# Optimization experiments

Hardware: AMD Instinct MI355X
Metric: run time of the kernel (lower is better)

Reference implementation:

```python
import jax, jax.numpy as jnp
import numpy as np

THRESH = 0.6
MIN_KEPT = 200000
FACTOR = 8
IGNORE_LABEL = -1


def _lin_coords(n_in, n_out):
    # scipy.ndimage.zoom (grid_mode=False): input_coord = i * (n_in-1)/(n_out-1)
    return jnp.linspace(0.0, n_in - 1.0, n_out)


def _zoom_bilinear(x, h_out, w_out):
    # x: (n, c, h, w) -> (n, c, h_out, w_out), separable order-1 (bilinear) zoom
    h, w = x.shape[-2], x.shape[-1]
    yc = _lin_coords(h, h_out)
    xc = _lin_coords(w, w_out)
    y0 = jnp.floor(yc).astype(jnp.int32)
    y1 = jnp.minimum(y0 + 1, h - 1)
    wy = (yc - y0)[None, None, :, None]
    x0 = jnp.floor(xc).astype(jnp.int32)
    x1 = jnp.minimum(x0 + 1, w - 1)
    wx = xc - x0
    a = jnp.take(x, y0, axis=2) * (1.0 - wy) + jnp.take(x, y1, axis=2) * wy
    return jnp.take(a, x0, axis=3) * (1.0 - wx) + jnp.take(a, x1, axis=3) * wx


def _zoom_nearest(t, h_out, w_out):
    # t: (n, h, w) int labels -> (n, h_out, w_out), order-0 (nearest) zoom
    h, w = t.shape[-2], t.shape[-1]
    yi = jnp.round(_lin_coords(h, h_out)).astype(jnp.int32)
    xi = jnp.round(_lin_coords(w, w_out)).astype(jnp.int32)
    return t[:, yi][:, :, xi]


def setup_inputs() -> dict:
    key = jax.random.key(0)
    k1, k2 = jax.random.split(key)
    predict = jax.random.normal(k1, (8, 19, 512, 1024), dtype=jnp.float32)
    target = jax.random.randint(k2, (8, 512, 1024), 0, 19, dtype=jnp.int32)
    return {"predict": predict, "target": target}


def reference(predict, target):
    n, c, h, w = predict.shape
    prob = jax.nn.softmax(predict, axis=1)  # (n, c, h, w)

    # ---- find_threshold: quantile on the factor-downsampled prediction ----
    h_s, w_s = int(round(h / FACTOR)), int(round(w / FACTOR))
    prob_s = _zoom_bilinear(prob, h_s, w_s)          # (n, c, h_s, w_s)
    tgt_s = _zoom_nearest(target, h_s, w_s)          # (n, h_s, w_s)
    # pred_s[i] = prob_s[n_i, label_i, y_i, x_i]
    pred_s = jnp.take_along_axis(prob_s, tgt_s[:, None].astype(jnp.int32), axis=1)[:, 0].ravel()
    min_kept_s = MIN_KEPT // (FACTOR * FACTOR)
    k_th = min(int(pred_s.shape[0]), min_kept_s) - 1  # static
    kth_val = jnp.sort(pred_s)[k_th]                  # == np.partition(pred, k_th)[k_th]
    threshold = jnp.where(kth_val > THRESH, kth_val, jnp.float32(THRESH))

    # ---- generate_new_target: keep hard pixels (pred prob <= threshold) ----
    pred_full = jnp.take_along_axis(prob, target[:, None].astype(jnp.int32), axis=1)[:, 0]  # (n, h, w)
    kept = (pred_full <= threshold) & (target >= 0)
    new_target = jnp.where(kept, target, IGNORE_LABEL)
    return new_target
```

## Files before the change

### kernel.cpp

```cpp
#include <hip/hip_runtime.h>
#include <math.h>

#define N_IMG 8
#define C_CH 19
#define H_IMG 512
#define W_IMG 1024
#define HW (H_IMG * W_IMG)
#define NDS (N_IMG * 64 * 128)
#define K_TH 3124
#define THRESH_F 0.6f

typedef float  f32x4 __attribute__((ext_vector_type(4)));
typedef int    i32x4 __attribute__((ext_vector_type(4)));

__global__ __launch_bounds__(256) void k0_zero(float* __restrict__ pred_s) {
    int idx = (blockIdx.x * 256 + threadIdx.x) * 4;
    *reinterpret_cast<f32x4*>(pred_s + idx) = (f32x4)(0.0f);
}

__global__ __launch_bounds__(256) void k1_fused(const float* __restrict__ predict,
                                                const int* __restrict__ target,
                                                float* __restrict__ pred_full,
                                                float* __restrict__ pred_s) {
    int tid = blockIdx.x * blockDim.x + threadIdx.x;
    int p = tid * 4;
    int n = p >> 19;
    int o = p & (HW - 1);
    int y = o >> 10;
    int xb = o & 1023;
    const float* base = predict + (size_t)n * C_CH * HW + o;

    i32x4 tg = *reinterpret_cast<const i32x4*>(target + p);

    f32x4 v[C_CH];
    f32x4 m = (f32x4)(-INFINITY);
    #pragma unroll
    for (int c = 0; c < C_CH; c++) {
        f32x4 x = __builtin_nontemporal_load(
            reinterpret_cast<const f32x4*>(base + (size_t)c * HW));
        v[c] = x;
        m.x = fmaxf(m.x, x.x); m.y = fmaxf(m.y, x.y);
        m.z = fmaxf(m.z, x.z); m.w = fmaxf(m.w, x.w);
    }
    f32x4 s = (f32x4)(0.0f);
    f32x4 et = (f32x4)(0.0f);
    #pragma unroll
    for (int c = 0; c < C_CH; c++) {
        float ex = expf(v[c].x - m.x);
        float ey = expf(v[c].y - m.y);
        float ez = expf(v[c].z - m.z);
        float ew = expf(v[c].w - m.w);
        s.x += ex; s.y += ey; s.z += ez; s.w += ew;
        if (c == tg.x) et.x = ex;
        if (c == tg.y) et.y = ey;
        if (c == tg.z) et.z = ez;
        if (c == tg.w) et.w = ew;
    }
    f32x4 pf;
    pf.x = et.x / s.x; pf.y = et.y / s.y; pf.z = et.z / s.z; pf.w = et.w / s.w;
    *reinterpret_cast<f32x4*>(pred_full + p) = pf;

    int jm[2]; float wym[2]; int yrow[2]; int nym = 0;
    {
        int jc = (int)((float)y * (63.0f / 511.0f));
        for (int dj = -1; dj <= 2; dj++) {
            int j = jc + dj;
            if (j < 0 || j > 63) continue;
            float yc = (float)j * (511.0f / 63.0f);
            int y0 = (int)yc;
            if (y0 > H_IMG - 1) y0 = H_IMG - 1;
            int y1 = min(y0 + 1, H_IMG - 1);
            float wy = yc - (float)y0;
            int yi = min((int)rintf(yc), H_IMG - 1);
            if (y0 == y && nym < 2) { jm[nym] = j; wym[nym] = 1.0f - wy; yrow[nym] = yi; nym++; }
            if (y1 == y && nym < 2) { jm[nym] = j; wym[nym] = wy;        yrow[nym] = yi; nym++; }
        }
    }
    if (nym) {
        #pragma unroll
        for (int k = 0; k < 4; k++) {
            int x = xb + k;
            int im[2]; float wxm[2]; int xcol[2]; int nxm = 0;
            int ic = (int)((float)x * (127.0f / 1023.0f));
            for (int di = -1; di <= 2; di++) {
                int i = ic + di;
                if (i < 0 || i > 127) continue;
                float xc = (float)i * (1023.0f / 127.0f);
                int x0 = (int)xc;
                if (x0 > W_IMG - 1) x0 = W_IMG - 1;
                int x1 = min(x0 + 1, W_IMG - 1);
                float wx = xc - (float)x0;
                int xi = min((int)rintf(xc), W_IMG - 1);
                if (x0 == x && nxm < 2) { im[nxm] = i; wxm[nxm] = 1.0f - wx; xcol[nxm] = xi; nxm++; }
                if (x1 == x && nxm < 2) { im[nxm] = i; wxm[nxm] = wx;        xcol[nxm] = xi; nxm++; }
            }
            for (int a = 0; a < nym; a++) {
                for (int b = 0; b < nxm; b++) {
                    int L = target[n * HW + yrow[a] * W_IMG + xcol[b]];
                    if (L < 0) L = 0;
                    float vL = v[0][k];
                    #pragma unroll
                    for (int c = 1; c < C_CH; c++) if (c == L) vL = v[c][k];
                    float e = expf(vL - m[k]);
                    float contrib = wym[a] * wxm[b] * (e / s[k]);
                    atomicAdd(&pred_s[n * 8192 + jm[a] * 128 + im[b]], contrib);
                }
            }
        }
    }
}

#define K2_THREADS 1024
#define K2_WAVES (K2_THREADS / 64)

__global__ __launch_bounds__(K2_THREADS) void k2_select(const float* __restrict__ pred_s,
                                                        float* __restrict__ thr_out) {
    __shared__ unsigned int hist[K2_WAVES * 2048];
    __shared__ unsigned int tot[2048];
    __shared__ unsigned int wsum[K2_WAVES];
    __shared__ unsigned int s_bin, s_k;

    const int t = threadIdx.x;
    const int lane = t & 63;
    const int wave = t >> 6;

    unsigned int prefix = 0;
    unsigned int k = K_TH;

    for (int lvl = 0; lvl < 3; lvl++) {
        const int nb = (lvl == 2) ? 1024 : 2048;

        for (int b = t; b < K2_WAVES * nb; b += K2_THREADS) hist[b] = 0;
        __syncthreads();

        unsigned int* myhist = &hist[wave * nb];
        for (int idx = t; idx < NDS; idx += K2_THREADS) {
            unsigned int u = __float_as_uint(pred_s[idx]);
            bool ok;
            unsigned int bin;
            if (lvl == 0)      { ok = true;                bin = u >> 21; }
            else if (lvl == 1) { ok = (u >> 21) == prefix; bin = (u >> 10) & 2047u; }
            else               { ok = (u >> 10) == prefix; bin = u & 1023u; }
            if (ok) atomicAdd(&myhist[bin], 1u);
        }
        __syncthreads();

        for (int b = t; b < nb; b += K2_THREADS) {
            unsigned int sm = 0;
            #pragma unroll
            for (int w = 0; w < K2_WAVES; w++) sm += hist[w * nb + b];
            tot[b] = sm;
        }
        __syncthreads();

        unsigned int c0, c1, s;
        if (nb == 2048) { c0 = tot[2 * t]; c1 = tot[2 * t + 1]; s = c0 + c1; }
        else            { c0 = tot[t];     c1 = 0;              s = c0; }

        unsigned int incl = s;
        #pragma unroll
        for (int off = 1; off < 64; off <<= 1) {
            unsigned int vv = (unsigned int)__shfl_up((int)incl, off, 64);
            if (lane >= off) incl += vv;
        }
        if (lane == 63) wsum[wave] = incl;
        __syncthreads();
        unsigned int woff = 0;
        for (int w = 0; w < wave; w++) woff += wsum[w];
        unsigned int excl = woff + incl - s;

        if (k >= excl && k < excl + s) {
            if (nb == 2048) {
                if (k < excl + c0) { s_bin = 2u * t;     s_k = k - excl; }
                else               { s_bin = 2u * t + 1; s_k = k - excl - c0; }
            } else {
                s_bin = (unsigned int)t; s_k = k - excl;
            }
        }
        __syncthreads();

        unsigned int b = s_bin;
        k = s_k;
        if (lvl == 0)      prefix = b;
        else if (lvl == 1) prefix = (prefix << 11) | b;
        else               prefix = (prefix << 10) | b;
        __syncthreads();
    }

    if (t == 0) {
        float kth = __uint_as_float(prefix);
        *thr_out = (kth > THRESH_F) ? kth : THRESH_F;
    }
}

__global__ __launch_bounds__(256) void k3_mask(const float* __restrict__ pred_full,
                                               const int* __restrict__ target,
                                               const float* __restrict__ thr_ptr,
                                               int* __restrict__ out) {
    int tid = blockIdx.x * blockDim.x + threadIdx.x;
    int p = tid * 4;
    f32x4 pf = *reinterpret_cast<const f32x4*>(pred_full + p);
    i32x4 tg = *reinterpret_cast<const i32x4*>(target + p);
    float thr = *thr_ptr;
    i32x4 r;
    r.x = (pf.x <= thr && tg.x >= 0) ? tg.x : -1;
    r.y = (pf.y <= thr && tg.y >= 0) ? tg.y : -1;
    r.z = (pf.z <= thr && tg.z >= 0) ? tg.z : -1;
    r.w = (pf.w <= thr && tg.w >= 0) ? tg.w : -1;
    __builtin_nontemporal_store(r, reinterpret_cast<i32x4*>(out + p));
}

extern "C" void kernel_launch(void* const* d_in, const int* in_sizes, int n_in,
                              void* d_out, int out_size, void* d_ws, size_t ws_size,
                              hipStream_t stream) {
    const float* predict = (const float*)d_in[0];
    const int* target    = (const int*)d_in[1];
    int* out = (int*)d_out;

    float* thr       = (float*)d_ws;
    float* pred_s    = (float*)((char*)d_ws + 4096);
    float* pred_full = (float*)((char*)d_ws + (1 << 20));

    hipLaunchKernelGGL(k0_zero, dim3(NDS / (256 * 4)), dim3(256), 0, stream, pred_s);
    hipLaunchKernelGGL(k1_fused, dim3(N_IMG * HW / (4 * 256)), dim3(256), 0, stream,
                       predict, target, pred_full, pred_s);
    hipLaunchKernelGGL(k2_select, dim3(1), dim3(K2_THREADS), 0, stream, pred_s, thr);
    hipLaunchKernelGGL(k3_mask, dim3(N_IMG * HW / (4 * 256)), dim3(256), 0, stream,
                       pred_full, target, thr, out);
}
```

Baseline: 472.8 us.

## Compute downsampled probabilities by direct gather instead of scatter atomics

Replaces the scatter-style accumulation, where full-resolution threads atomically added weighted contributions into the downsampled buffer, with dedicated gather blocks. Each gather thread recomputes softmax at its four bilinear source pixels and writes its downsampled value directly. This drops the zeroing kernel, the atomics and the per-pixel neighbour search in the main path. The cost is redundant softmax work on scattered, uncoalesced strided loads in the gather blocks. Those blocks come first in the grid and may delay the main blocks somewhat.

```diff
diff --git a/kernel.cpp b/kernel.cpp
--- a/kernel.cpp
+++ b/kernel.cpp
@@ -10,24 +10,73 @@
 #define K_TH 3124
 #define THRESH_F 0.6f
 
+#define GATHER_BLOCKS 256
+#define MAIN_BLOCKS (N_IMG * HW / (4 * 256))
+
 typedef float  f32x4 __attribute__((ext_vector_type(4)));
 typedef int    i32x4 __attribute__((ext_vector_type(4)));
-
-__global__ __launch_bounds__(256) void k0_zero(float* __restrict__ pred_s) {
-    int idx = (blockIdx.x * 256 + threadIdx.x) * 4;
-    *reinterpret_cast<f32x4*>(pred_s + idx) = (f32x4)(0.0f);
-}
 
 __global__ __launch_bounds__(256) void k1_fused(const float* __restrict__ predict,
                                                 const int* __restrict__ target,
                                                 float* __restrict__ pred_full,
                                                 float* __restrict__ pred_s) {
-    int tid = blockIdx.x * blockDim.x + threadIdx.x;
+    if (blockIdx.x < GATHER_BLOCKS) {
+        int gid = blockIdx.x * 256 + threadIdx.x;
+        int i = gid & 127;
+        int j = (gid >> 7) & 63;
+        int n = gid >> 13;
+
+        float yc = (float)j * (511.0f / 63.0f);
+        int y0 = (int)yc; if (y0 > H_IMG - 1) y0 = H_IMG - 1;
+        int y1 = min(y0 + 1, H_IMG - 1);
+        float wy = yc - (float)y0;
+        int yi = min((int)rintf(yc), H_IMG - 1);
+
+        float xc = (float)i * (1023.0f / 127.0f);
+        int x0 = (int)xc; if (x0 > W_IMG - 1) x0 = W_IMG - 1;
+        int x1 = min(x0 + 1, W_IMG - 1);
+        float wx = xc - (float)x0;
+        int xi = min((int)rintf(xc), W_IMG - 1);
+
+        int L = target[n * HW + yi * W_IMG + xi];
+        if (L < 0) L = 0;
+
+        const float* basep = predict + (size_t)n * C_CH * HW;
+        float p[2][2];
+        #pragma unroll
+        for (int a = 0; a < 2; a++) {
+            int y = a ? y1 : y0;
+            #pragma unroll
+            for (int b = 0; b < 2; b++) {
+                int x = b ? x1 : x0;
+                const float* bp = basep + y * W_IMG + x;
+                float v[C_CH];
+                float m = -INFINITY;
+                #pragma unroll
+                for (int c = 0; c < C_CH; c++) {
+                    v[c] = bp[(size_t)c * HW];
+                    m = fmaxf(m, v[c]);
+                }
+                float s = 0.0f, eL = 0.0f;
+                #pragma unroll
+                for (int c = 0; c < C_CH; c++) {
+                    float e = expf(v[c] - m);
+                    s += e;
+                    if (c == L) eL = e;
+                }
+                p[a][b] = eL / s;
+            }
+        }
+        float a0 = p[0][0] * (1.0f - wy) + p[1][0] * wy;
+        float a1 = p[0][1] * (1.0f - wy) + p[1][1] * wy;
+        pred_s[n * 8192 + j * 128 + i] = a0 * (1.0f - wx) + a1 * wx;
+        return;
+    }
+
+    int tid = (blockIdx.x - GATHER_BLOCKS) * 256 + threadIdx.x;
     int p = tid * 4;
     int n = p >> 19;
     int o = p & (HW - 1);
-    int y = o >> 10;
-    int xb = o & 1023;
     const float* base = predict + (size_t)n * C_CH * HW + o;
 
     i32x4 tg = *reinterpret_cast<const i32x4*>(target + p);
@@ -59,55 +108,6 @@
     f32x4 pf;
     pf.x = et.x / s.x; pf.y = et.y / s.y; pf.z = et.z / s.z; pf.w = et.w / s.w;
     *reinterpret_cast<f32x4*>(pred_full + p) = pf;
-
-    int jm[2]; float wym[2]; int yrow[2]; int nym = 0;
-    {
-        int jc = (int)((float)y * (63.0f / 511.0f));
-        for (int dj = -1; dj <= 2; dj++) {
-            int j = jc + dj;
-            if (j < 0 || j > 63) continue;
-            float yc = (float)j * (511.0f / 63.0f);
-            int y0 = (int)yc;
-            if (y0 > H_IMG - 1) y0 = H_IMG - 1;
-            int y1 = min(y0 + 1, H_IMG - 1);
-            float wy = yc - (float)y0;
-            int yi = min((int)rintf(yc), H_IMG - 1);
-            if (y0 == y && nym < 2) { jm[nym] = j; wym[nym] = 1.0f - wy; yrow[nym] = yi; nym++; }
-            if (y1 == y && nym < 2) { jm[nym] = j; wym[nym] = wy;        yrow[nym] = yi; nym++; }
-        }
-    }
-    if (nym) {
-        #pragma unroll
-        for (int k = 0; k < 4; k++) {
-            int x = xb + k;
-            int im[2]; float wxm[2]; int xcol[2]; int nxm = 0;
-            int ic = (int)((float)x * (127.0f / 1023.0f));
-            for (int di = -1; di <= 2; di++) {
-                int i = ic + di;
-                if (i < 0 || i > 127) continue;
-                float xc = (float)i * (1023.0f / 127.0f);
-                int x0 = (int)xc;
-                if (x0 > W_IMG - 1) x0 = W_IMG - 1;
-                int x1 = min(x0 + 1, W_IMG - 1);
-                float wx = xc - (float)x0;
-                int xi = min((int)rintf(xc), W_IMG - 1);
-                if (x0 == x && nxm < 2) { im[nxm] = i; wxm[nxm] = 1.0f - wx; xcol[nxm] = xi; nxm++; }
-                if (x1 == x && nxm < 2) { im[nxm] = i; wxm[nxm] = wx;        xcol[nxm] = xi; nxm++; }
-            }
-            for (int a = 0; a < nym; a++) {
-                for (int b = 0; b < nxm; b++) {
-                    int L = target[n * HW + yrow[a] * W_IMG + xcol[b]];
-                    if (L < 0) L = 0;
-                    float vL = v[0][k];
-                    #pragma unroll
-                    for (int c = 1; c < C_CH; c++) if (c == L) vL = v[c][k];
-                    float e = expf(vL - m[k]);
-                    float contrib = wym[a] * wxm[b] * (e / s[k]);
-                    atomicAdd(&pred_s[n * 8192 + jm[a] * 128 + im[b]], contrib);
-                }
-            }
-        }
-    }
 }
 
 #define K2_THREADS 1024
@@ -221,8 +221,7 @@
     float* pred_s    = (float*)((char*)d_ws + 4096);
     float* pred_full = (float*)((char*)d_ws + (1 << 20));
 
-    hipLaunchKernelGGL(k0_zero, dim3(NDS / (256 * 4)), dim3(256), 0, stream, pred_s);
-    hipLaunchKernelGGL(k1_fused, dim3(N_IMG * HW / (4 * 256)), dim3(256), 0, stream,
+    hipLaunchKernelGGL(k1_fused, dim3(GATHER_BLOCKS + MAIN_BLOCKS), dim3(256), 0, stream,
                        predict, target, pred_full, pred_s);
     hipLaunchKernelGGL(k2_select, dim3(1), dim3(K2_THREADS), 0, stream, pred_s, thr);
     hipLaunchKernelGGL(k3_mask, dim3(N_IMG * HW / (4 * 256)), dim3(256), 0, stream,
```

Result: slower. 483.3 us (+2.2%).

## Write speculative mask in softmax kernel and recompute only if threshold differs

Applied to the files above, without the earlier changes.

The fused softmax kernel now writes the final mask directly, using the default threshold, instead of storing per-pixel probabilities to a workspace. A fix-up kernel reads the selected threshold and returns early when it equals the default. Otherwise it recomputes softmax from the input and rewrites the mask. The selection kernel also caches its values in registers across the three radix passes instead of reloading them. This removes the intermediate probability buffer traffic, at the cost of a full recompute pass when the threshold is raised.

```diff
diff --git a/kernel.cpp b/kernel.cpp
--- a/kernel.cpp
+++ b/kernel.cpp
@@ -20,7 +20,7 @@
 
 __global__ __launch_bounds__(256) void k1_fused(const float* __restrict__ predict,
                                                 const int* __restrict__ target,
-                                                float* __restrict__ pred_full,
+                                                int* __restrict__ out,
                                                 float* __restrict__ pred_s) {
     int tid = blockIdx.x * blockDim.x + threadIdx.x;
     int p = tid * 4;
@@ -58,7 +58,13 @@
     }
     f32x4 pf;
     pf.x = et.x / s.x; pf.y = et.y / s.y; pf.z = et.z / s.z; pf.w = et.w / s.w;
-    *reinterpret_cast<f32x4*>(pred_full + p) = pf;
+
+    i32x4 r;
+    r.x = (pf.x <= THRESH_F && tg.x >= 0) ? tg.x : -1;
+    r.y = (pf.y <= THRESH_F && tg.y >= 0) ? tg.y : -1;
+    r.z = (pf.z <= THRESH_F && tg.z >= 0) ? tg.z : -1;
+    r.w = (pf.w <= THRESH_F && tg.w >= 0) ? tg.w : -1;
+    __builtin_nontemporal_store(r, reinterpret_cast<i32x4*>(out + p));
 
     int jm[2]; float wym[2]; int yrow[2]; int nym = 0;
     {
@@ -112,6 +118,7 @@
 
 #define K2_THREADS 1024
 #define K2_WAVES (K2_THREADS / 64)
+#define K2_PER_T (NDS / K2_THREADS)
 
 __global__ __launch_bounds__(K2_THREADS) void k2_select(const float* __restrict__ pred_s,
                                                         float* __restrict__ thr_out) {
@@ -124,6 +131,11 @@
     const int lane = t & 63;
     const int wave = t >> 6;
 
+    unsigned int u[K2_PER_T];
+    #pragma unroll
+    for (int r = 0; r < K2_PER_T; r++)
+        u[r] = __float_as_uint(pred_s[t + r * K2_THREADS]);
+
     unsigned int prefix = 0;
     unsigned int k = K_TH;
 
@@ -134,13 +146,14 @@
         __syncthreads();
 
         unsigned int* myhist = &hist[wave * nb];
-        for (int idx = t; idx < NDS; idx += K2_THREADS) {
-            unsigned int u = __float_as_uint(pred_s[idx]);
+        #pragma unroll
+        for (int r = 0; r < K2_PER_T; r++) {
+            unsigned int uu = u[r];
             bool ok;
             unsigned int bin;
-            if (lvl == 0)      { ok = true;                bin = u >> 21; }
-            else if (lvl == 1) { ok = (u >> 21) == prefix; bin = (u >> 10) & 2047u; }
-            else               { ok = (u >> 10) == prefix; bin = u & 1023u; }
+            if (lvl == 0)      { ok = true;                 bin = uu >> 21; }
+            else if (lvl == 1) { ok = (uu >> 21) == prefix; bin = (uu >> 10) & 2047u; }
+            else               { ok = (uu >> 10) == prefix; bin = uu & 1023u; }
             if (ok) atomicAdd(&myhist[bin], 1u);
         }
         __syncthreads();
@@ -155,7 +168,7 @@
 
         unsigned int c0, c1, s;
         if (nb == 2048) { c0 = tot[2 * t]; c1 = tot[2 * t + 1]; s = c0 + c1; }
-        else            { c0 = tot[t];     c1 = 0;              s = c0; }
+        else            { c0 = (t < 1024) ? tot[t] : 0u; c1 = 0; s = c0; }
 
         unsigned int incl = s;
         #pragma unroll
@@ -169,7 +182,7 @@
         for (int w = 0; w < wave; w++) woff += wsum[w];
         unsigned int excl = woff + incl - s;
 
-        if (k >= excl && k < excl + s) {
+        if (s && k >= excl && k < excl + s) {
             if (nb == 2048) {
                 if (k < excl + c0) { s_bin = 2u * t;     s_k = k - excl; }
                 else               { s_bin = 2u * t + 1; s_k = k - excl - c0; }
@@ -193,21 +206,50 @@
     }
 }
 
-__global__ __launch_bounds__(256) void k3_mask(const float* __restrict__ pred_full,
-                                               const int* __restrict__ target,
-                                               const float* __restrict__ thr_ptr,
-                                               int* __restrict__ out) {
+__global__ __launch_bounds__(256) void k3_fix(const float* __restrict__ predict,
+                                              const int* __restrict__ target,
+                                              const float* __restrict__ thr_ptr,
+                                              int* __restrict__ out) {
+    float thr = *thr_ptr;
+    if (thr == THRESH_F) return;
+
     int tid = blockIdx.x * blockDim.x + threadIdx.x;
     int p = tid * 4;
-    f32x4 pf = *reinterpret_cast<const f32x4*>(pred_full + p);
+    int n = p >> 19;
+    int o = p & (HW - 1);
+    const float* base = predict + (size_t)n * C_CH * HW + o;
+
     i32x4 tg = *reinterpret_cast<const i32x4*>(target + p);
-    float thr = *thr_ptr;
+
+    f32x4 v[C_CH];
+    f32x4 m = (f32x4)(-INFINITY);
+    #pragma unroll
+    for (int c = 0; c < C_CH; c++) {
+        f32x4 x = *reinterpret_cast<const f32x4*>(base + (size_t)c * HW);
+        v[c] = x;
+        m.x = fmaxf(m.x, x.x); m.y = fmaxf(m.y, x.y);
+        m.z = fmaxf(m.z, x.z); m.w = fmaxf(m.w, x.w);
+    }
+    f32x4 s = (f32x4)(0.0f);
+    f32x4 et = (f32x4)(0.0f);
+    #pragma unroll
+    for (int c = 0; c < C_CH; c++) {
+        float ex = expf(v[c].x - m.x);
+        float ey = expf(v[c].y - m.y);
+        float ez = expf(v[c].z - m.z);
+        float ew = expf(v[c].w - m.w);
+        s.x += ex; s.y += ey; s.z += ez; s.w += ew;
+        if (c == tg.x) et.x = ex;
+        if (c == tg.y) et.y = ey;
+        if (c == tg.z) et.z = ez;
+        if (c == tg.w) et.w = ew;
+    }
     i32x4 r;
-    r.x = (pf.x <= thr && tg.x >= 0) ? tg.x : -1;
-    r.y = (pf.y <= thr && tg.y >= 0) ? tg.y : -1;
-    r.z = (pf.z <= thr && tg.z >= 0) ? tg.z : -1;
-    r.w = (pf.w <= thr && tg.w >= 0) ? tg.w : -1;
-    __builtin_nontemporal_store(r, reinterpret_cast<i32x4*>(out + p));
+    r.x = (et.x / s.x <= thr && tg.x >= 0) ? tg.x : -1;
+    r.y = (et.y / s.y <= thr && tg.y >= 0) ? tg.y : -1;
+    r.z = (et.z / s.z <= thr && tg.z >= 0) ? tg.z : -1;
+    r.w = (et.w / s.w <= thr && tg.w >= 0) ? tg.w : -1;
+    *reinterpret_cast<i32x4*>(out + p) = r;
 }
 
 extern "C" void kernel_launch(void* const* d_in, const int* in_sizes, int n_in,
@@ -217,14 +259,13 @@
     const int* target    = (const int*)d_in[1];
     int* out = (int*)d_out;
 
-    float* thr       = (float*)d_ws;
-    float* pred_s    = (float*)((char*)d_ws + 4096);
-    float* pred_full = (float*)((char*)d_ws + (1 << 20));
+    float* thr    = (float*)d_ws;
+    float* pred_s = (float*)((char*)d_ws + 4096);
 
     hipLaunchKernelGGL(k0_zero, dim3(NDS / (256 * 4)), dim3(256), 0, stream, pred_s);
     hipLaunchKernelGGL(k1_fused, dim3(N_IMG * HW / (4 * 256)), dim3(256), 0, stream,
-                       predict, target, pred_full, pred_s);
+                       predict, target, out, pred_s);
     hipLaunchKernelGGL(k2_select, dim3(1), dim3(K2_THREADS), 0, stream, pred_s, thr);
-    hipLaunchKernelGGL(k3_mask, dim3(N_IMG * HW / (4 * 256)), dim3(256), 0, stream,
-                       pred_full, target, thr, out);
-}
+    hipLaunchKernelGGL(k3_fix, dim3(N_IMG * HW / (4 * 256)), dim3(256), 0, stream,
+                       predict, target, thr, out);
+}
```

Result: slower. 523.9 us (+10.8%).
